# Optimization experiments

Measured on AMD Instinct MI355X. Metric: run time of the kernel, lower is better.

## Reference

```python
import math
import jax, jax.numpy as jnp
import numpy as np

B, T, C = 2, 2048, 1024
NH = 16
HS = C // NH
WIN = 256

def setup_inputs() -> dict:
    key = jax.random.key(0)
    k1, k2, k3 = jax.random.split(key, 3)
    x = jax.random.normal(k1, (B, T, C), dtype=jnp.float32)
    # Linear weights stored as (in, out) so y = x @ W
    scale_attn = 1.0 / math.sqrt(C)
    W_attn = jax.random.normal(k2, (C, 3 * C), dtype=jnp.float32) * scale_attn
    W_proj = jax.random.normal(k3, (C, C), dtype=jnp.float32) * scale_attn
    return {"x": x, "W_attn": W_attn, "W_proj": W_proj}

def reference(x, W_attn, W_proj):
    Bs, Ts, Cs = x.shape
    W = min(WIN, Ts)
    qkv = x @ W_attn                                  # [B,T,3C]
    q, k, v = jnp.split(qkv, 3, axis=-1)
    # [B,T,C] -> [B,NH,T,HS]
    q = q.reshape(Bs, Ts, NH, HS).transpose(0, 2, 1, 3)
    k = k.reshape(Bs, Ts, NH, HS).transpose(0, 2, 1, 3)
    v = v.reshape(Bs, Ts, NH, HS).transpose(0, 2, 1, 3)
    att = jnp.einsum('bhqd,bhkd->bhqk', q, k) * (1.0 / math.sqrt(HS))
    i_idx = jnp.arange(Ts)[:, None]
    j_idx = jnp.arange(Ts)[None, :]
    mask = (j_idx <= i_idx) & (i_idx - j_idx < W)      # causal sliding window
    att = jnp.where(mask[None, None, :, :], att, -jnp.inf)
    att = jax.nn.softmax(att, axis=-1)
    y = jnp.einsum('bhqk,bhkd->bhqd', att, v)          # [B,NH,T,HS]
    y = y.transpose(0, 2, 1, 3).reshape(Bs, Ts, Cs)
    return y @ W_proj
```

## Files before the change

### kernel.cpp

```cpp
#include <hip/hip_runtime.h>
#include <hip/hip_bf16.h>
#include <cstdint>

#define B_   2
#define T_   2048
#define C_   1024
#define NH_  16
#define HS_  64
#define WIN_ 256
#define M_   (B_*T_)

typedef __attribute__((ext_vector_type(8)))  short          short8;
typedef __attribute__((ext_vector_type(8)))  unsigned short ushortx8;
typedef __attribute__((ext_vector_type(8)))  __bf16         bf16x8;
typedef __attribute__((ext_vector_type(4)))  float          floatx4;
typedef __attribute__((ext_vector_type(16))) float          floatx16;

__device__ __forceinline__ unsigned short f2bf(float f) {
    union { float f; uint32_t u; } v; v.f = f;
    uint32_t r = (v.u + 0x7FFFu + ((v.u >> 16) & 1u)) >> 16;
    return (unsigned short)r;
}

__device__ __forceinline__ floatx4 mfma16(short8 a, short8 b, floatx4 c) {
    return __builtin_amdgcn_mfma_f32_16x16x32_bf16(
        __builtin_bit_cast(bf16x8, a), __builtin_bit_cast(bf16x8, b), c, 0, 0, 0);
}
__device__ __forceinline__ floatx16 mfma32(short8 a, short8 b, floatx16 c) {
    return __builtin_amdgcn_mfma_f32_32x32x16_bf16(
        __builtin_bit_cast(bf16x8, a), __builtin_bit_cast(bf16x8, b), c, 0, 0, 0);
}

__device__ __forceinline__ void async16(const void* g, void* l) {
    __builtin_amdgcn_global_load_lds(
        (const __attribute__((address_space(1))) void*)g,
        (__attribute__((address_space(3))) void*)l, 16, 0, 0);
}

#define NB_CONV 4096
#define NB_WA   768
#define NB_WP   256

__device__ void transpose_tile(const float* __restrict__ in, unsigned short* __restrict__ out,
                               int K, int N, int kt, int nt, unsigned short (*tile)[65])
{
    const int k0 = kt * 64, n0 = nt * 64;
    const int tr = threadIdx.x >> 4;
    const int tc = (threadIdx.x & 15) * 4;
    #pragma unroll
    for (int it = 0; it < 4; it++) {
        int row = tr + it * 16;
        float4 v = *(const float4*)&in[(size_t)(k0 + row) * N + n0 + tc];
        tile[row][tc + 0] = f2bf(v.x);
        tile[row][tc + 1] = f2bf(v.y);
        tile[row][tc + 2] = f2bf(v.z);
        tile[row][tc + 3] = f2bf(v.w);
    }
    __syncthreads();
    #pragma unroll
    for (int it = 0; it < 4; it++) {
        int nrow = tr + it * 16;
        ushort4 h;
        h.x = tile[tc + 0][nrow]; h.y = tile[tc + 1][nrow];
        h.z = tile[tc + 2][nrow]; h.w = tile[tc + 3][nrow];
        *(ushort4*)&out[(size_t)(n0 + nrow) * K + k0 + tc] = h;
    }
}

__global__ __launch_bounds__(256)
void prep_kernel(const float* __restrict__ x, const float* __restrict__ W_attn,
                 const float* __restrict__ W_proj,
                 unsigned short* __restrict__ xb, unsigned short* __restrict__ Wa_t,
                 unsigned short* __restrict__ Wp_t)
{
    __shared__ unsigned short tile[64][65];
    const int bid = blockIdx.x;
    if (bid < NB_CONV) {
        int i = (bid * 256 + threadIdx.x) * 4;
        float4 v = *(const float4*)&x[i];
        ushort4 h;
        h.x = f2bf(v.x); h.y = f2bf(v.y); h.z = f2bf(v.z); h.w = f2bf(v.w);
        *(ushort4*)&xb[i] = h;
    } else if (bid < NB_CONV + NB_WA) {
        int idx = bid - NB_CONV;
        transpose_tile(W_attn, Wa_t, C_, 3 * C_, idx / 48, idx % 48, tile);
    } else {
        int idx = bid - NB_CONV - NB_WA;
        transpose_tile(W_proj, Wp_t, C_, C_, idx / 16, idx % 16, tile);
    }
}

template<int MT, bool OUT_BF16, bool VSPLIT>
__global__ __launch_bounds__(256)
void gemm32(const unsigned short* __restrict__ A,
            const unsigned short* __restrict__ Bt,
            void* __restrict__ Cp, unsigned short* __restrict__ vt,
            int M, int N, int K)
{
    constexpr int BK = 64;
    constexpr int BM = 64 * MT;
    __shared__ unsigned short As[BM * BK];
    __shared__ unsigned short Bs[128 * BK];

    const int tid  = threadIdx.x;
    const int lane = tid & 63;
    const int wave = tid >> 6;
    const int l32  = lane & 31;
    const int hi   = lane >> 5;
    const int px   = l32 & 7;
    const int wm   = (wave & 1) * 32 * MT;
    const int wn   = (wave >> 1) * 64;
    const int m0   = blockIdx.y * BM;
    const int n0   = blockIdx.x * 128;

    const int ri = lane >> 3;
    const int pg = lane & 7;
    const int gg = pg ^ ri;

    floatx16 acc[MT][2];
    #pragma unroll
    for (int i = 0; i < MT; i++)
        #pragma unroll
        for (int j = 0; j < 2; j++) acc[i][j] = (floatx16)(0.f);

    const unsigned short* gA = &A[(size_t)(m0 + wave * 8 + ri) * K + gg * 8];
    const unsigned short* gB = &Bt[(size_t)(n0 + wave * 8 + ri) * K + gg * 8];
    unsigned short* lA = &As[(wave * 8) * BK];
    unsigned short* lB = &Bs[(wave * 8) * BK];

    for (int k0 = 0; k0 < K; k0 += BK) {
        #pragma unroll
        for (int s = 0; s < 2 * MT; s++)
            async16(gA + k0 + (size_t)s * 32 * K, lA + s * 32 * BK);
        #pragma unroll
        for (int s = 0; s < 4; s++)
            async16(gB + k0 + (size_t)s * 32 * K, lB + s * 32 * BK);
        __syncthreads();

        #pragma unroll
        for (int ks = 0; ks < 4; ks++) {
            short8 af[MT], bfr[2];
            #pragma unroll
            for (int i = 0; i < MT; i++) {
                int r = wm + i * 32 + l32;
                int p = (ks * 2 + hi) ^ px;
                af[i] = *(const short8*)(&As[r * BK + p * 8]);
            }
            #pragma unroll
            for (int j = 0; j < 2; j++) {
                int r = wn + j * 32 + l32;
                int p = (ks * 2 + hi) ^ px;
                bfr[j] = *(const short8*)(&Bs[r * BK + p * 8]);
            }
            #pragma unroll
            for (int i = 0; i < MT; i++)
                #pragma unroll
                for (int j = 0; j < 2; j++)
                    acc[i][j] = mfma32(af[i], bfr[j], acc[i][j]);
        }
        __syncthreads();
    }

    #pragma unroll
    for (int i = 0; i < MT; i++)
        #pragma unroll
        for (int j = 0; j < 2; j++) {
            const int col  = n0 + wn + j * 32 + l32;
            const int row0 = m0 + wm + i * 32 + 4 * hi;
            if (VSPLIT && col >= 2 * C_) {
                const int hd = col - 2 * C_;
                const int hh = hd >> 6, d = hd & 63;
                #pragma unroll
                for (int g = 0; g < 4; g++) {
                    int rowg = row0 + 8 * g;
                    int bb = rowg >> 11, t = rowg & (T_ - 1);
                    ushort4 h4;
                    h4.x = f2bf(acc[i][j][g * 4 + 0]);
                    h4.y = f2bf(acc[i][j][g * 4 + 1]);
                    h4.z = f2bf(acc[i][j][g * 4 + 2]);
                    h4.w = f2bf(acc[i][j][g * 4 + 3]);
                    *(ushort4*)&vt[((size_t)(bb * NH_ + hh) * 64 + d) * T_ + t] = h4;
                }
            } else {
                #pragma unroll
                for (int g = 0; g < 4; g++)
                    #pragma unroll
                    for (int rr = 0; rr < 4; rr++) {
                        int row = row0 + 8 * g + rr;
                        if (OUT_BF16)
                            ((unsigned short*)Cp)[(size_t)row * N + col] = f2bf(acc[i][j][g * 4 + rr]);
                        else
                            ((float*)Cp)[(size_t)row * N + col] = acc[i][j][g * 4 + rr];
                    }
            }
        }
}

__global__ __launch_bounds__(256)
void attn_kernel(const unsigned short* __restrict__ qkv,
                 const unsigned short* __restrict__ vt,
                 unsigned short* __restrict__ y)
{
    __shared__ unsigned short Ps[4][16 * 72];

    const int tid  = threadIdx.x;
    const int lane = tid & 63;
    const int wave = tid >> 6;
    const int l16  = lane & 15;
    const int quad = lane >> 4;

    const int q0 = blockIdx.x * 64 + wave * 16;
    const int h  = blockIdx.y;
    const int b  = blockIdx.z;
    const size_t base = (size_t)b * T_;
    const int ROW  = 3 * C_;
    const int qoff = h * HS_;
    const int koff = C_ + h * HS_;
    const size_t vbase = ((size_t)(b * NH_ + h) * 64) * T_;
    const float SC = 0.125f * 1.44269504f;

    short8 aq[2];
    #pragma unroll
    for (int ks = 0; ks < 2; ks++)
        aq[ks] = *(const short8*)&qkv[(base + q0 + l16) * ROW + qoff + ks * 32 + quad * 8];

    floatx4 O[4];
    #pragma unroll
    for (int j = 0; j < 4; j++) O[j] = (floatx4){0.f, 0.f, 0.f, 0.f};
    float psum[4] = {0.f, 0.f, 0.f, 0.f};

    int kb_lo = q0 - (WIN_ - 1);
    kb_lo = (kb_lo > 0 ? kb_lo : 0) & ~63;
    const int kb_hi = blockIdx.x * 64;

    for (int kb = kb_lo; kb <= kb_hi; kb += 64) {
        floatx4 s[4];
        #pragma unroll
        for (int nt = 0; nt < 4; nt++) s[nt] = (floatx4){0.f, 0.f, 0.f, 0.f};
        #pragma unroll
        for (int ks = 0; ks < 2; ks++)
            #pragma unroll
            for (int nt = 0; nt < 4; nt++) {
                short8 bk = *(const short8*)&qkv[(base + kb + nt * 16 + l16) * ROW
                                                 + koff + ks * 32 + quad * 8];
                s[nt] = mfma16(aq[ks], bk, s[nt]);
            }

        #pragma unroll
        for (int nt = 0; nt < 4; nt++)
            #pragma unroll
            for (int r = 0; r < 4; r++) {
                int dist = (q0 + quad * 4 + r) - (kb + nt * 16 + l16);
                float sv = ((unsigned)dist < (unsigned)WIN_) ? s[nt][r] * SC : -1e30f;
                float e = exp2f(sv);
                psum[r] += e;
                s[nt][r] = e;
            }

        #pragma unroll
        for (int nt = 0; nt < 4; nt++)
            #pragma unroll
            for (int r = 0; r < 4; r++)
                Ps[wave][(quad * 4 + r) * 72 + nt * 16 + l16] = f2bf(s[nt][r]);

        #pragma unroll
        for (int ks = 0; ks < 2; ks++) {
            short8 ap = *(const short8*)&Ps[wave][l16 * 72 + ks * 32 + quad * 8];
            #pragma unroll
            for (int jt = 0; jt < 4; jt++) {
                short8 bv = *(const short8*)&vt[vbase + (size_t)(jt * 16 + l16) * T_
                                                + kb + ks * 32 + quad * 8];
                O[jt] = mfma16(ap, bv, O[jt]);
            }
        }
    }

    #pragma unroll
    for (int r = 0; r < 4; r++) {
        #pragma unroll
        for (int off = 8; off >= 1; off >>= 1)
            psum[r] += __shfl_xor(psum[r], off, 64);
    }

    #pragma unroll
    for (int jt = 0; jt < 4; jt++)
        #pragma unroll
        for (int r = 0; r < 4; r++)
            Ps[wave][(quad * 4 + r) * 72 + jt * 16 + l16] = f2bf(O[jt][r] / psum[r]);
    #pragma unroll
    for (int it = 0; it < 2; it++) {
        int c = lane + 64 * it;
        int qr = c >> 3, dc = (c & 7) * 8;
        *(ushortx8*)&y[(base + q0 + qr) * C_ + qoff + dc] =
            *(const ushortx8*)&Ps[wave][qr * 72 + dc];
    }
}

extern "C" void kernel_launch(void* const* d_in, const int* in_sizes, int n_in,
                              void* d_out, int out_size, void* d_ws, size_t ws_size,
                              hipStream_t stream)
{
    const float* x      = (const float*)d_in[0];
    const float* W_attn = (const float*)d_in[1];
    const float* W_proj = (const float*)d_in[2];
    float* out = (float*)d_out;

    unsigned short* xb   = (unsigned short*)d_ws;
    unsigned short* Wa_t = xb   + (size_t)M_ * C_;
    unsigned short* Wp_t = Wa_t + (size_t)3 * C_ * C_;
    unsigned short* qkv  = Wp_t + (size_t)C_ * C_;
    unsigned short* y    = qkv  + (size_t)M_ * 3 * C_;
    unsigned short* vtg  = y    + (size_t)M_ * C_;

    dim3 blk(256);
    prep_kernel<<<NB_CONV + NB_WA + NB_WP, blk, 0, stream>>>(x, W_attn, W_proj, xb, Wa_t, Wp_t);
    gemm32<2, true, true><<<dim3((3 * C_) / 128, M_ / 128), blk, 0, stream>>>(
        xb, Wa_t, qkv, vtg, M_, 3 * C_, C_);
    attn_kernel<<<dim3(T_ / 64, NH_, B_), blk, 0, stream>>>(qkv, vtg, y);
    gemm32<1, false, false><<<dim3(C_ / 128, M_ / 64), blk, 0, stream>>>(
        y, Wp_t, out, nullptr, M_, C_, C_);
}
```

Before: 173.9 us.

## Double-buffer K fragments in attention and remap blocks to a 1D grid

The attention loop now prefetches the next K tile into registers (ping-pong buffers) while the current tile is computed, and loads V fragments before each tile's compute. This hides global-load latency. The grid is flattened to 1D, with a swizzle that groups 8 head/batch slices per query tile so neighbouring blocks share K/V in L2. It costs extra registers, which may lower occupancy.

Result: no change. 173.9 us (+0.0%).

```diff
diff --git a/kernel.cpp b/kernel.cpp
--- a/kernel.cpp
+++ b/kernel.cpp
@@ -196,6 +196,70 @@
         }
 }
 
+__device__ __forceinline__ void load_kf(short8 kf[8], const unsigned short* kbase,
+                                        int l16, int quad)
+{
+    #pragma unroll
+    for (int nt = 0; nt < 4; nt++)
+        #pragma unroll
+        for (int ks = 0; ks < 2; ks++)
+            kf[nt * 2 + ks] = *(const short8*)&kbase[(size_t)(nt * 16 + l16) * (3 * C_)
+                                                     + ks * 32 + quad * 8];
+}
+
+__device__ __forceinline__ void load_vf(short8 vf[8], const unsigned short* vbase,
+                                        int l16, int quad)
+{
+    #pragma unroll
+    for (int jt = 0; jt < 4; jt++)
+        #pragma unroll
+        for (int ks = 0; ks < 2; ks++)
+            vf[jt * 2 + ks] = *(const short8*)&vbase[(size_t)(jt * 16 + l16) * T_
+                                                     + ks * 32 + quad * 8];
+}
+
+__device__ __forceinline__ void attn_tile(const short8 aq[2], const short8 kf[8],
+                                          const short8 vf[8], int kb, int q0,
+                                          int l16, int quad,
+                                          unsigned short* Pstrip,
+                                          floatx4 O[4], float psum[4])
+{
+    const float SC = 0.125f * 1.44269504f;
+    floatx4 s[4];
+    #pragma unroll
+    for (int nt = 0; nt < 4; nt++) s[nt] = (floatx4){0.f, 0.f, 0.f, 0.f};
+    #pragma unroll
+    for (int ks = 0; ks < 2; ks++)
+        #pragma unroll
+        for (int nt = 0; nt < 4; nt++)
+            s[nt] = mfma16(aq[ks], kf[nt * 2 + ks], s[nt]);
+
+    #pragma unroll
+    for (int nt = 0; nt < 4; nt++)
+        #pragma unroll
+        for (int r = 0; r < 4; r++) {
+            int dist = (q0 + quad * 4 + r) - (kb + nt * 16 + l16);
+            float sv = ((unsigned)dist < (unsigned)WIN_) ? s[nt][r] * SC : -1e30f;
+            float e = exp2f(sv);
+            psum[r] += e;
+            s[nt][r] = e;
+        }
+
+    #pragma unroll
+    for (int nt = 0; nt < 4; nt++)
+        #pragma unroll
+        for (int r = 0; r < 4; r++)
+            Pstrip[(quad * 4 + r) * 72 + nt * 16 + l16] = f2bf(s[nt][r]);
+
+    #pragma unroll
+    for (int ks = 0; ks < 2; ks++) {
+        short8 ap = *(const short8*)&Pstrip[l16 * 72 + ks * 32 + quad * 8];
+        #pragma unroll
+        for (int jt = 0; jt < 4; jt++)
+            O[jt] = mfma16(ap, vf[jt * 2 + ks], O[jt]);
+    }
+}
+
 __global__ __launch_bounds__(256)
 void attn_kernel(const unsigned short* __restrict__ qkv,
                  const unsigned short* __restrict__ vt,
@@ -209,15 +273,20 @@
     const int l16  = lane & 15;
     const int quad = lane >> 4;
 
-    const int q0 = blockIdx.x * 64 + wave * 16;
-    const int h  = blockIdx.y;
-    const int b  = blockIdx.z;
+    const int g  = blockIdx.x;
+    const int yq = g >> 3;
+    const int hb = (g & 7) + 8 * (yq >> 5);
+    const int qt = yq & 31;
+    const int h  = hb & 15;
+    const int b  = hb >> 4;
+
+    const int q0 = qt * 64 + wave * 16;
     const size_t base = (size_t)b * T_;
     const int ROW  = 3 * C_;
     const int qoff = h * HS_;
     const int koff = C_ + h * HS_;
     const size_t vbase = ((size_t)(b * NH_ + h) * 64) * T_;
-    const float SC = 0.125f * 1.44269504f;
+    unsigned short* Pstrip = Ps[wave];
 
     short8 aq[2];
     #pragma unroll
@@ -231,48 +300,36 @@
 
     int kb_lo = q0 - (WIN_ - 1);
     kb_lo = (kb_lo > 0 ? kb_lo : 0) & ~63;
-    const int kb_hi = blockIdx.x * 64;
-
-    for (int kb = kb_lo; kb <= kb_hi; kb += 64) {
-        floatx4 s[4];
-        #pragma unroll
-        for (int nt = 0; nt < 4; nt++) s[nt] = (floatx4){0.f, 0.f, 0.f, 0.f};
-        #pragma unroll
-        for (int ks = 0; ks < 2; ks++)
-            #pragma unroll
-            for (int nt = 0; nt < 4; nt++) {
-                short8 bk = *(const short8*)&qkv[(base + kb + nt * 16 + l16) * ROW
-                                                 + koff + ks * 32 + quad * 8];
-                s[nt] = mfma16(aq[ks], bk, s[nt]);
-            }
-
-        #pragma unroll
-        for (int nt = 0; nt < 4; nt++)
-            #pragma unroll
-            for (int r = 0; r < 4; r++) {
-                int dist = (q0 + quad * 4 + r) - (kb + nt * 16 + l16);
-                float sv = ((unsigned)dist < (unsigned)WIN_) ? s[nt][r] * SC : -1e30f;
-                float e = exp2f(sv);
-                psum[r] += e;
-                s[nt][r] = e;
-            }
-
-        #pragma unroll
-        for (int nt = 0; nt < 4; nt++)
-            #pragma unroll
-            for (int r = 0; r < 4; r++)
-                Ps[wave][(quad * 4 + r) * 72 + nt * 16 + l16] = f2bf(s[nt][r]);
-
-        #pragma unroll
-        for (int ks = 0; ks < 2; ks++) {
-            short8 ap = *(const short8*)&Ps[wave][l16 * 72 + ks * 32 + quad * 8];
-            #pragma unroll
-            for (int jt = 0; jt < 4; jt++) {
-                short8 bv = *(const short8*)&vt[vbase + (size_t)(jt * 16 + l16) * T_
-                                                + kb + ks * 32 + quad * 8];
-                O[jt] = mfma16(ap, bv, O[jt]);
-            }
-        }
+    const int kb_hi = qt * 64;
+
+    const unsigned short* kgb = &qkv[base * ROW + koff];
+    const unsigned short* vgb = &vt[vbase];
+
+    short8 ka[8], kbb[8];
+    load_kf(ka, kgb + (size_t)kb_lo * ROW, l16, quad);
+
+    int kb = kb_lo;
+    while (kb + 64 <= kb_hi) {
+        load_kf(kbb, kgb + (size_t)(kb + 64) * ROW, l16, quad);
+        {
+            short8 vf[8];
+            load_vf(vf, vgb + kb, l16, quad);
+            attn_tile(aq, ka, vf, kb, q0, l16, quad, Pstrip, O, psum);
+        }
+        kb += 64;
+        if (kb + 64 <= kb_hi)
+            load_kf(ka, kgb + (size_t)(kb + 64) * ROW, l16, quad);
+        {
+            short8 vf[8];
+            load_vf(vf, vgb + kb, l16, quad);
+            attn_tile(aq, kbb, vf, kb, q0, l16, quad, Pstrip, O, psum);
+        }
+        kb += 64;
+    }
+    if (kb <= kb_hi) {
+        short8 vf[8];
+        load_vf(vf, vgb + kb, l16, quad);
+        attn_tile(aq, ka, vf, kb, q0, l16, quad, Pstrip, O, psum);
     }
 
     #pragma unroll
@@ -286,13 +343,13 @@
     for (int jt = 0; jt < 4; jt++)
         #pragma unroll
         for (int r = 0; r < 4; r++)
-            Ps[wave][(quad * 4 + r) * 72 + jt * 16 + l16] = f2bf(O[jt][r] / psum[r]);
+            Pstrip[(quad * 4 + r) * 72 + jt * 16 + l16] = f2bf(O[jt][r] / psum[r]);
     #pragma unroll
     for (int it = 0; it < 2; it++) {
         int c = lane + 64 * it;
         int qr = c >> 3, dc = (c & 7) * 8;
         *(ushortx8*)&y[(base + q0 + qr) * C_ + qoff + dc] =
-            *(const ushortx8*)&Ps[wave][qr * 72 + dc];
+            *(const ushortx8*)&Pstrip[qr * 72 + dc];
     }
 }
 
@@ -316,7 +373,7 @@
     prep_kernel<<<NB_CONV + NB_WA + NB_WP, blk, 0, stream>>>(x, W_attn, W_proj, xb, Wa_t, Wp_t);
     gemm32<2, true, true><<<dim3((3 * C_) / 128, M_ / 128), blk, 0, stream>>>(
         xb, Wa_t, qkv, vtg, M_, 3 * C_, C_);
-    attn_kernel<<<dim3(T_ / 64, NH_, B_), blk, 0, stream>>>(qkv, vtg, y);
+    attn_kernel<<<(T_ / 64) * NH_ * B_, blk, 0, stream>>>(qkv, vtg, y);
     gemm32<1, false, false><<<dim3(C_ / 128, M_ / 64), blk, 0, stream>>>(
         y, Wp_t, out, nullptr, M_, C_, C_);
 }
```

## Stage K and V tiles in swizzled shared memory and remap attention grid

Applied to the files above, without the earlier changes.

The attention kernel now loads each 64-key K and V tile once per block into LDS with async copies and an XOR swizzle, and all four waves read from it. Before, each wave fetched the same K/V fragments from global memory on its own. The launch becomes a 1D grid, remapped so that consecutive blocks cover different heads for the same query tile, which may improve cache locality. The cost is two barriers per key tile and extra LDS use, with no double buffering, so load latency is not overlapped.

After: 152.3 us (median of 2 runs). 1.14x faster.

```diff
diff --git a/kernel.cpp b/kernel.cpp
--- a/kernel.cpp
+++ b/kernel.cpp
@@ -201,6 +201,8 @@
                  const unsigned short* __restrict__ vt,
                  unsigned short* __restrict__ y)
 {
+    __shared__ unsigned short Ks[64 * 64];
+    __shared__ unsigned short Vs[64 * 64];
     __shared__ unsigned short Ps[4][16 * 72];
 
     const int tid  = threadIdx.x;
@@ -208,32 +210,53 @@
     const int wave = tid >> 6;
     const int l16  = lane & 15;
     const int quad = lane >> 4;
-
-    const int q0 = blockIdx.x * 64 + wave * 16;
-    const int h  = blockIdx.y;
-    const int b  = blockIdx.z;
+    const int sw   = l16 & 7;
+
+    const int g  = blockIdx.x;
+    const int yq = g >> 3;
+    const int hb = (g & 7) + 8 * (yq >> 5);
+    const int qt = yq & 31;
+    const int h  = hb & 15;
+    const int b  = hb >> 4;
+
+    const int q0b = qt * 64;
+    const int q0w = q0b + wave * 16;
     const size_t base = (size_t)b * T_;
     const int ROW  = 3 * C_;
     const int qoff = h * HS_;
     const int koff = C_ + h * HS_;
     const size_t vbase = ((size_t)(b * NH_ + h) * 64) * T_;
+    unsigned short* Pstrip = Ps[wave];
     const float SC = 0.125f * 1.44269504f;
 
+    const int ri = lane >> 3;
+    const int gg = (lane & 7) ^ ri;
+
     short8 aq[2];
     #pragma unroll
     for (int ks = 0; ks < 2; ks++)
-        aq[ks] = *(const short8*)&qkv[(base + q0 + l16) * ROW + qoff + ks * 32 + quad * 8];
+        aq[ks] = *(const short8*)&qkv[(base + q0w + l16) * ROW + qoff + ks * 32 + quad * 8];
 
     floatx4 O[4];
     #pragma unroll
     for (int j = 0; j < 4; j++) O[j] = (floatx4){0.f, 0.f, 0.f, 0.f};
     float psum[4] = {0.f, 0.f, 0.f, 0.f};
 
-    int kb_lo = q0 - (WIN_ - 1);
+    int kb_lo = q0b - (WIN_ - 1);
     kb_lo = (kb_lo > 0 ? kb_lo : 0) & ~63;
-    const int kb_hi = blockIdx.x * 64;
-
-    for (int kb = kb_lo; kb <= kb_hi; kb += 64) {
+
+    for (int kb = kb_lo; kb <= q0b; kb += 64) {
+        __syncthreads();
+        #pragma unroll
+        for (int c = 0; c < 2; c++) {
+            int row = wave * 16 + c * 8;
+            async16(&qkv[(base + kb + row + ri) * ROW + koff + gg * 8],
+                    &Ks[row * 64]);
+            async16(&vt[vbase + (size_t)(row + ri) * T_ + kb + gg * 8],
+                    &Vs[row * 64]);
+        }
+        __syncthreads();
+
         floatx4 s[4];
         #pragma unroll
         for (int nt = 0; nt < 4; nt++) s[nt] = (floatx4){0.f, 0.f, 0.f, 0.f};
@@ -241,8 +264,8 @@
         for (int ks = 0; ks < 2; ks++)
             #pragma unroll
             for (int nt = 0; nt < 4; nt++) {
-                short8 bk = *(const short8*)&qkv[(base + kb + nt * 16 + l16) * ROW
-                                                 + koff + ks * 32 + quad * 8];
+                short8 bk = *(const short8*)&Ks[(nt * 16 + l16) * 64
+                                                + (((ks * 4 + quad) ^ sw) * 8)];
                 s[nt] = mfma16(aq[ks], bk, s[nt]);
             }
 
@@ -250,7 +273,7 @@
         for (int nt = 0; nt < 4; nt++)
             #pragma unroll
             for (int r = 0; r < 4; r++) {
-                int dist = (q0 + quad * 4 + r) - (kb + nt * 16 + l16);
+                int dist = (q0w + quad * 4 + r) - (kb + nt * 16 + l16);
                 float sv = ((unsigned)dist < (unsigned)WIN_) ? s[nt][r] * SC : -1e30f;
                 float e = exp2f(sv);
                 psum[r] += e;
@@ -261,15 +284,15 @@
         for (int nt = 0; nt < 4; nt++)
             #pragma unroll
             for (int r = 0; r < 4; r++)
-                Ps[wave][(quad * 4 + r) * 72 + nt * 16 + l16] = f2bf(s[nt][r]);
+                Pstrip[(quad * 4 + r) * 72 + nt * 16 + l16] = f2bf(s[nt][r]);
 
         #pragma unroll
         for (int ks = 0; ks < 2; ks++) {
-            short8 ap = *(const short8*)&Ps[wave][l16 * 72 + ks * 32 + quad * 8];
+            short8 ap = *(const short8*)&Pstrip[l16 * 72 + ks * 32 + quad * 8];
             #pragma unroll
             for (int jt = 0; jt < 4; jt++) {
-                short8 bv = *(const short8*)&vt[vbase + (size_t)(jt * 16 + l16) * T_
-                                                + kb + ks * 32 + quad * 8];
+                short8 bv = *(const short8*)&Vs[(jt * 16 + l16) * 64
+                                                + (((ks * 4 + quad) ^ sw) * 8)];
                 O[jt] = mfma16(ap, bv, O[jt]);
             }
         }
@@ -286,13 +309,13 @@
     for (int jt = 0; jt < 4; jt++)
         #pragma unroll
         for (int r = 0; r < 4; r++)
-            Ps[wave][(quad * 4 + r) * 72 + jt * 16 + l16] = f2bf(O[jt][r] / psum[r]);
+            Pstrip[(quad * 4 + r) * 72 + jt * 16 + l16] = f2bf(O[jt][r] / psum[r]);
     #pragma unroll
     for (int it = 0; it < 2; it++) {
         int c = lane + 64 * it;
         int qr = c >> 3, dc = (c & 7) * 8;
-        *(ushortx8*)&y[(base + q0 + qr) * C_ + qoff + dc] =
-            *(const ushortx8*)&Ps[wave][qr * 72 + dc];
+        *(ushortx8*)&y[(base + q0w + qr) * C_ + qoff + dc] =
+            *(const ushortx8*)&Pstrip[qr * 72 + dc];
     }
 }
 
@@ -316,7 +339,7 @@
     prep_kernel<<<NB_CONV + NB_WA + NB_WP, blk, 0, stream>>>(x, W_attn, W_proj, xb, Wa_t, Wp_t);
     gemm32<2, true, true><<<dim3((3 * C_) / 128, M_ / 128), blk, 0, stream>>>(
         xb, Wa_t, qkv, vtg, M_, 3 * C_, C_);
-    attn_kernel<<<dim3(T_ / 64, NH_, B_), blk, 0, stream>>>(qkv, vtg, y);
+    attn_kernel<<<(T_ / 64) * NH_ * B_, blk, 0, stream>>>(qkv, vtg, y);
     gemm32<1, false, false><<<dim3(C_ / 128, M_ / 64), blk, 0, stream>>>(
         y, Wp_t, out, nullptr, M_, C_, C_);
 }
```
